# Kernel tuning notes

Hardware: AMD Instinct MI355X
Metric: run time of the kernel (lower is better)

The kernel has to match this reference:

```python
import jax, jax.numpy as jnp
import numpy as np

N_QUBITS = 12
N_LAYERS = 3
FEAT_DIM = 64
BATCH = 8192
PI = float(np.pi)


def setup_inputs() -> dict:
    key = jax.random.key(0)
    k1, k2, k3 = jax.random.split(key, 3)
    x = jax.random.normal(k1, (BATCH, FEAT_DIM), dtype=jnp.float32)
    # nn.Linear(feature_dim, num_qubits, bias=False) weight: [num_qubits, feature_dim]
    W = jax.random.normal(k2, (N_QUBITS, FEAT_DIM), dtype=jnp.float32) * (1.0 / np.sqrt(FEAT_DIM))
    # quantum params ~ Uniform(-pi, pi), shape [num_layers, num_qubits, 2] (RY, RZ angles)
    quantum_params = jax.random.uniform(k3, (N_LAYERS, N_QUBITS, 2), minval=-PI, maxval=PI, dtype=jnp.float32)
    return {"x": x, "W": W, "quantum_params": quantum_params}


def _halves(st, ax):
    a0 = jax.lax.index_in_dim(st, 0, ax, keepdims=True)
    a1 = jax.lax.index_in_dim(st, 1, ax, keepdims=True)
    return a0, a1


def _ry(st, theta, q, n):
    # RY(t) = [[cos t/2, -sin t/2], [sin t/2, cos t/2]] on qubit q (wire 0 = most significant)
    ax = q + 1
    c = jnp.cos(theta * 0.5)
    s = jnp.sin(theta * 0.5)
    if jnp.ndim(c) > 0:  # per-batch angles -> broadcast [B,1,...,1]
        c = c.reshape(c.shape + (1,) * n)
        s = s.reshape(s.shape + (1,) * n)
    a0, a1 = _halves(st, ax)
    return jnp.concatenate([c * a0 - s * a1, s * a0 + c * a1], axis=ax)


def _rz(st, theta, q, n):
    # RZ(t) = diag(e^{-i t/2}, e^{i t/2}) on qubit q
    ax = q + 1
    ph = jnp.exp(-0.5j * theta)
    a0, a1 = _halves(st, ax)
    return jnp.concatenate([ph * a0, jnp.conj(ph) * a1], axis=ax)


def _cnot(st, ctrl, tgt):
    # flip target amplitudes on the control=1 subspace
    ax_c, ax_t = ctrl + 1, tgt + 1
    s0, s1 = _halves(st, ax_c)
    return jnp.concatenate([s0, jnp.flip(s1, axis=ax_t)], axis=ax_c)


def reference(x, W, quantum_params):
    n = N_QUBITS
    # feature projection + tanh squashing to [-pi, pi]
    angles = jnp.tanh(x @ W.T) * PI  # [B, n]
    B = x.shape[0]
    # batched state vector |0...0>, shape [B] + [2]*n (wire 0 most significant, PennyLane convention)
    st = jnp.zeros((B,) + (2,) * n, dtype=jnp.complex64)
    st = st.at[(slice(None),) + (0,) * n].set(1.0)
    for layer in range(N_LAYERS):
        # data (re)uploading: RY(features[i]) each layer since data_reuploading=True
        for q in range(n):
            st = _ry(st, angles[:, q], q, n)
        # variational rotations
        for q in range(n):
            st = _ry(st, quantum_params[layer, q, 0], q, n)
            st = _rz(st, quantum_params[layer, q, 1], q, n)
        # ring entanglement
        for q in range(n):
            st = _cnot(st, q, (q + 1) % n)
    probs = jnp.real(st * jnp.conj(st))  # [B] + [2]*n
    outs = []
    for q in range(n):  # <PauliZ_q> = p(bit_q=0) - p(bit_q=1)
        axes = tuple(a for a in range(1, n + 1) if a != q + 1)
        p = probs.sum(axis=axes)  # [B, 2]
        outs.append(p[:, 0] - p[:, 1])
    return jnp.stack(outs, axis=1).astype(x.dtype)  # [B, n]
```

## Files before the change

kernel.cpp:

```cpp
#include <hip/hip_runtime.h>

namespace {

constexpr int NQ = 12;
constexpr int NL = 3;
constexpr int FEAT = 64;
constexpr float PI_F = 3.14159265358979323846f;

typedef float f2 __attribute__((ext_vector_type(2)));

constexpr int par12(unsigned x) { int p = 0; for (int i = 0; i < 12; ++i) p ^= (int)((x >> i) & 1u); return p; }
constexpr int lead12(unsigned x) { for (int k = 11; k >= 0; --k) if ((x >> k) & 1u) return k; return -1; }

struct Ech { unsigned v[16] = {}; int n = 0; };
constexpr unsigned ech_reduce(const Ech& E, unsigned x) {
  for (int i = 0; i < E.n; ++i) { int lb = lead12(E.v[i]); if (lb >= 0 && ((x >> lb) & 1u)) x ^= E.v[i]; }
  return x;
}
constexpr bool ech_add(Ech& E, unsigned x) {
  unsigned r = ech_reduce(E, x);
  if (!r) return false;
  int lb = lead12(r);
  int pos = E.n;
  for (int i = 0; i < E.n; ++i) { if (lead12(E.v[i]) < lb) { pos = i; break; } }
  for (int i = E.n; i > pos; --i) E.v[i] = E.v[i - 1];
  E.v[pos] = r; E.n++;
  return true;
}

constexpr unsigned apmat(const unsigned* rows, unsigned v) {
  unsigned o = 0; for (int k = 0; k < 12; ++k) if (par12(rows[k] & v)) o |= 1u << k; return o;
}
constexpr bool inv12(const unsigned* in, unsigned* out) {
  unsigned a[12] = {}, b[12] = {};
  for (int k = 0; k < 12; ++k) { a[k] = in[k]; b[k] = 1u << k; }
  for (int c = 0; c < 12; ++c) {
    int p = -1;
    for (int r = c; r < 12; ++r) if ((a[r] >> c) & 1u) { p = r; break; }
    if (p < 0) return false;
    unsigned t = a[c]; a[c] = a[p]; a[p] = t; t = b[c]; b[c] = b[p]; b[p] = t;
    for (int r = 0; r < 12; ++r) if (r != c && ((a[r] >> c) & 1u)) { a[r] ^= a[c]; b[r] ^= b[c]; }
  }
  for (int k = 0; k < 12; ++k) out[k] = b[k];
  return true;
}
constexpr unsigned dropb(unsigned x, int t) {
  unsigned lm = (1u << t) - 1u;
  return (x & lm) | ((x >> 1) & (0x7FFu & ~lm));
}

struct Logical {
  unsigned m[NL][NQ] = {}, rv[NL][NQ] = {}, rf[NQ] = {};
  bool ok = false;
};
constexpr Logical compute_raw() {
  Logical mp{};
  unsigned col[NQ] = {}, row[NQ] = {};
  for (int b = 0; b < NQ; ++b) { col[b] = 1u << b; row[b] = 1u << b; }
  mp.ok = true;
  for (int L = 0; L < NL; ++L) {
    for (int q = 0; q < NQ; ++q) {
      mp.m[L][q]  = col[NQ - 1 - q];
      mp.rv[L][q] = row[NQ - 1 - q];
      if (par12(mp.m[L][q] & mp.rv[L][q]) != 1) mp.ok = false;
    }
    for (int q = 0; q < NQ; ++q) {
      int bc = NQ - 1 - q;
      int bt = NQ - 1 - ((q + 1) % NQ);
      col[bc] ^= col[bt];
      row[bt] ^= row[bc];
    }
  }
  for (int q = 0; q < NQ; ++q) mp.rf[q] = row[NQ - 1 - q];
  return mp;
}

struct Plan {
  unsigned l0m[NQ] = {}, l0r[NQ] = {};
  unsigned gm[4][6] = {};
  unsigned gr[4][6] = {};
  unsigned rf[NQ] = {};
  unsigned phi[4][6] = {};
  unsigned coffE[4][64] = {};
  int cb[4] = {};
  bool ok = false;
};

constexpr bool findH(const Ech& G, unsigned rho, unsigned& out) {
  for (unsigned t = 0; t < 12; ++t) {
    unsigned v = 1u << t;
    if (par12(v & rho) == 0 && ech_reduce(G, v)) { out = v; return true; }
  }
  for (unsigned v = 1; v < 4096u; ++v) {
    if (par12(v & rho) == 0 && ech_reduce(G, v)) { out = v; return true; }
  }
  return false;
}

constexpr Plan build_plan() {
  Logical raw = compute_raw();
  Plan P{};
  P.ok = raw.ok;
  for (int q = 0; q < NQ; ++q) { P.l0m[q] = raw.m[0][q]; P.l0r[q] = raw.rv[0][q]; }
  unsigned fwd[12] = {}, invc[12] = {};
  for (int k = 0; k < 12; ++k) { fwd[k] = 1u << k; invc[k] = 1u << k; }
  for (int ph = 0; ph < 4; ++ph) {
    const int L = 1 + ph / 2, q0 = (ph % 2) * 6;
    unsigned ml[6] = {};
    for (int i = 0; i < 6; ++i) ml[i] = raw.m[L][q0 + i];
    bool done = false;
    for (int cbi = 5; cbi >= 0 && !done; --cbi) {
      unsigned rho = fwd[6 + cbi];
      bool bad = false;
      int idx = -1;
      for (int i = 0; i < 6; ++i) if (par12(ml[i] & rho)) { idx = i; break; }
      unsigned uc = 0;
      Ech W{};
      if (idx >= 0) {
        uc = ml[idx];
        for (int i = 0; i < 6; ++i) {
          if (i == idx) continue;
          unsigned w = par12(ml[i] & rho) ? (ml[i] ^ uc) : ml[i];
          ech_add(W, w);
        }
        if (W.n > 5) bad = true;
      } else {
        for (int i = 0; i < 6; ++i) ech_add(W, ml[i]);
        if (W.n > 5) bad = true;
        if (!bad) {
          bool got = false;
          for (unsigned t = 0; t < 12 && !got; ++t) {
            unsigned v = 1u << t;
            if (par12(v & rho)) { uc = v; got = true; }
          }
          if (!got) bad = true;
        }
      }
      if (bad) continue;
      Ech G{};
      for (int i = 0; i < W.n && !bad; ++i) if (!ech_add(G, W.v[i])) bad = true;
      if (!bad && !ech_add(G, uc)) bad = true;
      if (bad) continue;
      unsigned regH[5] = {};
      int nH = W.n;
      for (int i = 0; i < nH; ++i) regH[i] = W.v[i];
      for (int slot = nH; slot < 5 && !bad; ++slot) {
        unsigned v = 0;
        if (!findH(G, rho, v)) { bad = true; break; }
        regH[slot] = v; ech_add(G, v);
      }
      if (bad) continue;
      unsigned lam[6] = {};
      for (int j = 0; j < 6 && !bad; ++j) {
        unsigned cand = invc[j];
        if (par12(cand & rho) != 0 || !ech_reduce(G, cand)) {
          if (!findH(G, rho, cand)) { bad = true; break; }
        }
        lam[j] = cand; ech_add(G, cand);
      }
      if (bad) continue;
      unsigned ncols[12] = {};
      for (int j = 0; j < 6; ++j) ncols[j] = lam[j];
      {
        int w = 0;
        for (int k = 0; k < 6; ++k) ncols[6 + k] = (k == cbi) ? uc : regH[w++];
      }
      unsigned Mrows[12] = {};
      for (int k = 0; k < 12; ++k) {
        unsigned r = 0;
        for (int j = 0; j < 12; ++j) r |= ((ncols[j] >> k) & 1u) << j;
        Mrows[k] = r;
      }
      unsigned fnew[12] = {};
      if (!inv12(Mrows, fnew)) continue;
      bool okp = true;
      unsigned gmv[6] = {}, grv[6] = {};
      for (int i = 0; i < 6 && okp; ++i) {
        unsigned SM = apmat(fnew, ml[i]);
        if (SM & 63u) okp = false;
        unsigned sg = 0;
        for (int k = 0; k < 12; ++k) if (par12(raw.rv[L][q0 + i] & ncols[k])) sg |= 1u << k;
        if (par12(SM & sg) != 1) okp = false;
        gmv[i] = SM; grv[i] = sg;
      }
      unsigned phj[6] = {}, Ust[6] = {};
      for (int j = 0; j < 6 && okp; ++j) {
        phj[j] = apmat(fwd, lam[j]);
        if ((phj[j] >> (6 + cbi)) & 1u) okp = false;
      }
      for (int k = 0; k < 6 && okp; ++k) {
        Ust[k] = apmat(fwd, ncols[6 + k]);
        if (((Ust[k] >> (6 + cbi)) & 1u) != (unsigned)(k == cbi ? 1 : 0)) okp = false;
      }
      if (!okp) continue;
      P.cb[ph] = cbi;
      for (int j = 0; j < 6; ++j) P.phi[ph][j] = phj[j];
      for (int rp = 0; rp < 64; ++rp) {
        unsigned psi = 0;
        for (int i = 0; i < 6; ++i) if ((rp >> i) & 1) psi ^= Ust[i];
        P.coffE[ph][rp] = dropb(psi, 6 + cbi);
      }
      for (int i = 0; i < 6; ++i) { P.gm[ph][i] = gmv[i]; P.gr[ph][i] = grv[i]; }
      for (int k = 0; k < 12; ++k) { fwd[k] = fnew[k]; invc[k] = ncols[k]; }
      done = true;
    }
    if (!done) { P.ok = false; return P; }
  }
  for (int q = 0; q < NQ; ++q) {
    unsigned sg = 0;
    for (int k = 0; k < 12; ++k) if (par12(raw.rf[q] & invc[k])) sg |= 1u << k;
    P.rf[q] = sg;
  }
  return P;
}

constexpr Plan PLAN = build_plan();
static_assert(PLAN.ok, "plan construction failed");

__device__ __forceinline__ f2 shuf(f2 a) { return __builtin_shufflevector(a, a, 1, 0); }

template<bool REAL>
__device__ __forceinline__ f2 updv(f2 a, f2 p, f2 arr, f2 aii, f2 brr, f2 bii) {
  f2 t = a * arr;
  if constexpr (!REAL) t = shuf(a) * aii + t;
  t = p * brr + t;
  if constexpr (!REAL) t = shuf(p) * bii + t;
  return t;
}
__device__ __forceinline__ f2 cmulv(f2 a, f2 urr, f2 uri) {
  return shuf(a) * uri + a * urr;
}

template<unsigned MLO>
__device__ __forceinline__ float shx(float v, int lane4) {
  if constexpr (MLO == 0u) {
    return v;
  } else if constexpr (MLO < 32u) {
    constexpr int off = (int)((MLO << 10) | 0x1fu);
    return __int_as_float(__builtin_amdgcn_ds_swizzle(__float_as_int(v), off));
  } else {
    int addr = lane4 ^ (int)(MLO << 2);
    return __int_as_float(__builtin_amdgcn_ds_bpermute(addr, __float_as_int(v)));
  }
}

template<unsigned M, unsigned R, int NREG, bool REAL>
__device__ __forceinline__ void gate(f2* st, float ghalf, float phihalf, int lane, int lane4) {
  float s, c;
  __sincosf(ghalf, &s, &c);
  constexpr unsigned MHI = (M >> 6) & 63u;
  constexpr unsigned MLO = M & 63u;
  constexpr unsigned RHI = (R >> 6) & 63u;
  constexpr unsigned RLO = R & 63u;
  float sL = (__popc((int)(RLO & (unsigned)lane)) & 1) ? -1.f : 1.f;
  float ar, aiS, brS, b0i;
  if constexpr (REAL) {
    ar = c; aiS = 0.f; brS = -s * sL; b0i = 0.f;
  } else {
    float sf, cf;
    __sincosf(phihalf, &sf, &cf);
    ar = c * cf; aiS = (-c * sf) * sL; brS = (-s * cf) * sL; b0i = s * sf;
  }
  f2 arr; arr.x = ar; arr.y = ar;
  f2 aip; aip.x = -aiS; aip.y = aiS;
  f2 aim; aim.x = aiS;  aim.y = -aiS;
  f2 brp; brp.x = brS;  brp.y = brS;
  f2 brm; brm.x = -brS; brm.y = -brS;
  f2 bii; bii.x = -b0i; bii.y = b0i;
  if constexpr (MLO == 0u) {
    constexpr unsigned TB = MHI & (~MHI + 1u);
    #pragma unroll
    for (int r = 0; r < NREG; ++r) {
      if ((r & (int)TB) == 0) {
        int r2 = r ^ (int)MHI;
        const bool rp = ((__builtin_popcount((unsigned)r & RHI)) & 1) != 0;
        f2 a = st[r], b = st[r2];
        st[r]  = rp ? updv<REAL>(a, b, arr, aim, brm, bii) : updv<REAL>(a, b, arr, aip, brp, bii);
        st[r2] = rp ? updv<REAL>(b, a, arr, aip, brp, bii) : updv<REAL>(b, a, arr, aim, brm, bii);
      }
    }
  } else {
    #pragma unroll
    for (int r = 0; r < NREG; ++r) {
      f2 p;
      p.x = shx<MLO>(st[r].x, lane4);
      p.y = shx<MLO>(st[r].y, lane4);
      const bool rp = ((__builtin_popcount((unsigned)r & RHI)) & 1) != 0;
      st[r] = rp ? updv<REAL>(st[r], p, arr, aim, brm, bii) : updv<REAL>(st[r], p, arr, aip, brp, bii);
    }
  }
}

template<int Q>
__device__ __forceinline__ void l0_lane(f2* st, const float* ang, const float* __restrict__ qp, int lane, int lane4) {
  if constexpr (Q < NQ) {
    constexpr unsigned M = PLAN.l0m[Q];
    if constexpr (M < 64u) {
      gate<M, PLAN.l0r[Q], 1, false>(st, 0.5f * (ang[Q] + qp[Q * 2 + 0]), 0.5f * qp[Q * 2 + 1], lane, lane4);
    }
    l0_lane<Q + 1>(st, ang, qp, lane, lane4);
  }
}
template<int Q, unsigned DONE>
__device__ __forceinline__ void l0_reg(f2* st, const float* ang, const float* __restrict__ qp) {
  if constexpr (Q < NQ) {
    constexpr unsigned M = PLAN.l0m[Q];
    if constexpr (M >= 64u) {
      constexpr unsigned TB = (M >> 6) & 63u;
      float sh = 0.5f * (ang[Q] + qp[Q * 2 + 0]);
      float ph = 0.5f * qp[Q * 2 + 1];
      float s, c, sf, cf;
      __sincosf(sh, &s, &c);
      __sincosf(ph, &sf, &cf);
      f2 u0r; u0r.x = c * cf;  u0r.y = c * cf;
      f2 u0i; u0i.x = c * sf;  u0i.y = -c * sf;
      f2 u1r; u1r.x = s * cf;  u1r.y = s * cf;
      f2 u1i; u1i.x = -s * sf; u1i.y = s * sf;
      #pragma unroll
      for (int r = 0; r < 64; ++r) {
        if ((r & ~(int)DONE & 63) == 0) {
          f2 a = st[r];
          int r2 = r | (int)TB;
          st[r]  = cmulv(a, u0r, u0i);
          st[r2] = cmulv(a, u1r, u1i);
        }
      }
      l0_reg<Q + 1, DONE | TB>(st, ang, qp);
    } else {
      l0_reg<Q + 1, DONE>(st, ang, qp);
    }
  }
}

__device__ __forceinline__ int pad(int a) { return a + (a >> 5); }

template<int PH>
__device__ __forceinline__ void remap(f2* st, f2* lds, int lane) {
  constexpr int b = PLAN.cb[PH];
  constexpr unsigned LM6 = (1u << b) - 1u;
  constexpr unsigned LM = (1u << (6 + b)) - 1u;
  unsigned B = 0;
  #pragma unroll
  for (int j = 0; j < 6; ++j) B ^= (unsigned)(-(int)((lane >> j) & 1)) & PLAN.phi[PH][j];
  unsigned rBe = (B & LM) | ((B >> 1) & (0x7FFu & ~LM));
  #pragma unroll
  for (int s = 0; s < 2; ++s) {
    #pragma unroll
    for (int r = 0; r < 64; ++r) {
      if (((r >> b) & 1) == s) {
        const int cr = (r & (int)LM6) | ((r >> 1) & (31 & ~(int)LM6));
        lds[pad((cr << 6) | lane)] = st[r];
      }
    }
    asm volatile("s_waitcnt lgkmcnt(0)" ::: "memory");
    #pragma unroll
    for (int rp = 0; rp < 64; ++rp) {
      if (((rp >> b) & 1) == s) {
        st[rp] = lds[pad((int)(rBe ^ PLAN.coffE[PH][rp]))];
      }
    }
    asm volatile("s_waitcnt lgkmcnt(0)" ::: "memory");
  }
}

template<int PH, int I>
__device__ __forceinline__ void do_phase(f2* st, const float* ang, const float* __restrict__ qp, int lane, int lane4) {
  if constexpr (I < 6) {
    constexpr int L = 1 + PH / 2;
    constexpr bool REAL = (L == NL - 1);
    constexpr int q = (PH % 2) * 6 + I;
    constexpr unsigned M = PLAN.gm[PH][I];
    constexpr unsigned R = PLAN.gr[PH][I];
    float th0 = qp[(L * NQ + q) * 2 + 0];
    float ph1 = REAL ? 0.f : 0.5f * qp[(L * NQ + q) * 2 + 1];
    gate<M, R, 64, REAL>(st, 0.5f * (ang[q] + th0), ph1, lane, lane4);
    do_phase<PH, I + 1>(st, ang, qp, lane, lane4);
  }
}

__device__ __forceinline__ float redsum(float v, int lane4) {
  v += shx<1>(v, lane4);
  v += shx<2>(v, lane4);
  v += shx<4>(v, lane4);
  v += shx<8>(v, lane4);
  v += shx<16>(v, lane4);
  v += shx<32>(v, lane4);
  return v;
}
__device__ __forceinline__ float fast_tanh(float x) {
  float e = __expf(2.f * x);
  float r = __builtin_amdgcn_rcpf(e + 1.f);
  return 1.f - 2.f * r;
}

template<int Q>
__device__ __forceinline__ void finish(const f2* acc6, float& outv, int lane, int lane4) {
  if constexpr (Q < NQ) {
    constexpr unsigned RLO = PLAN.rf[Q] & 63u;
    float a = (Q & 1) ? acc6[Q / 2].y : acc6[Q / 2].x;
    float sLn = (__popc((int)(RLO & (unsigned)lane)) & 1) ? -a : a;
    float t = redsum(sLn, lane4);
    if (lane == Q) outv = t;
    finish<Q + 1>(acc6, outv, lane, lane4);
  }
}

__global__ __launch_bounds__(64, 2) void qtr_kernel(const float* __restrict__ x,
                                                    const float* __restrict__ W,
                                                    const float* __restrict__ qp,
                                                    float* __restrict__ out) {
  __shared__ f2 ldsb[2112];
  int b = blockIdx.x;
  int lane = threadIdx.x;
  int lane4 = lane << 2;

  float xv = x[b * FEAT + lane];
  float ang[NQ];
  #pragma unroll
  for (int q = 0; q < NQ; ++q) {
    float prod = redsum(xv * W[q * FEAT + lane], lane4);
    ang[q] = PI_F * fast_tanh(prod);
  }

  f2 st[64];
  st[0].x = (lane == 0) ? 1.f : 0.f;
  st[0].y = 0.f;

  l0_lane<0>(st, ang, qp, lane, lane4);
  l0_reg<0, 0u>(st, ang, qp);

  remap<0>(st, ldsb, lane);
  do_phase<0, 0>(st, ang, qp, lane, lane4);
  remap<1>(st, ldsb, lane);
  do_phase<1, 0>(st, ang, qp, lane, lane4);
  remap<2>(st, ldsb, lane);
  do_phase<2, 0>(st, ang, qp, lane, lane4);
  remap<3>(st, ldsb, lane);
  do_phase<3, 0>(st, ang, qp, lane, lane4);

  f2 acc6[6];
  #pragma unroll
  for (int j = 0; j < 6; ++j) { acc6[j].x = 0.f; acc6[j].y = 0.f; }
  #pragma unroll
  for (int r = 0; r < 64; ++r) {
    f2 q2 = st[r] * st[r];
    float p = q2.x + q2.y;
    f2 pp; pp.x = p; pp.y = p;
    #pragma unroll
    for (int j = 0; j < 6; ++j) {
      const bool n0 = ((__builtin_popcount(((PLAN.rf[2 * j]     >> 6) & 63u) & (unsigned)r)) & 1) != 0;
      const bool n1 = ((__builtin_popcount(((PLAN.rf[2 * j + 1] >> 6) & 63u) & (unsigned)r)) & 1) != 0;
      f2 sg; sg.x = n0 ? -1.f : 1.f; sg.y = n1 ? -1.f : 1.f;
      acc6[j] = pp * sg + acc6[j];
    }
  }

  float outv = 0.f;
  finish<0>(acc6, outv, lane, lane4);

  if (lane < NQ) out[b * NQ + lane] = outv;
}

}

extern "C" void kernel_launch(void* const* d_in, const int* in_sizes, int n_in,
                              void* d_out, int out_size, void* d_ws, size_t ws_size,
                              hipStream_t stream) {
  const float* x  = (const float*)d_in[0];
  const float* W  = (const float*)d_in[1];
  const float* qp = (const float*)d_in[2];
  float* out = (float*)d_out;
  qtr_kernel<<<8192, 64, 0, stream>>>(x, W, qp, out);
}
```

Measured before the change: 129.4 us.

## Switch register state to split real/imag planes paired on a chosen register bit

Stores the 64 complex amplitudes per lane as 32 real and 32 imaginary float2 pairs, each pair holding the two values of a chosen register bit. Gates then run as packed FMAs on whole pairs instead of intra-vector swaps, and the LDS remaps pack and unpack between the layouts. The register bit is picked per phase to minimise in-pair swaps. This aims to raise packed-FMA use and drop shuffle overhead, but adds more complex remap code and may raise register pressure.

Result: slower. 133.7 us (+3.3%).

```diff
diff --git a/kernel.cpp b/kernel.cpp
--- a/kernel.cpp
+++ b/kernel.cpp
@@ -48,6 +48,8 @@
   unsigned lm = (1u << t) - 1u;
   return (x & lm) | ((x >> 1) & (0x7FFu & ~lm));
 }
+constexpr int drop6(int r, int c) { int lm = (1 << c) - 1; return (r & lm) | ((r >> 1) & (31 & ~lm)); }
+constexpr int ins6(int p, int slot, int c) { int lm = (1 << c) - 1; return (p & lm) | ((p & ~lm) << 1) | (slot << c); }
 
 struct Logical {
   unsigned m[NL][NQ] = {}, rv[NL][NQ] = {}, rf[NQ] = {};
@@ -217,19 +219,26 @@
 constexpr Plan PLAN = build_plan();
 static_assert(PLAN.ok, "plan construction failed");
 
-__device__ __forceinline__ f2 shuf(f2 a) { return __builtin_shufflevector(a, a, 1, 0); }
-
-template<bool REAL>
-__device__ __forceinline__ f2 updv(f2 a, f2 p, f2 arr, f2 aii, f2 brr, f2 bii) {
-  f2 t = a * arr;
-  if constexpr (!REAL) t = shuf(a) * aii + t;
-  t = p * brr + t;
-  if constexpr (!REAL) t = shuf(p) * bii + t;
-  return t;
-}
-__device__ __forceinline__ f2 cmulv(f2 a, f2 urr, f2 uri) {
-  return shuf(a) * uri + a * urr;
-}
+constexpr int pick_cp(int ph) {
+  int best = -1, bestCost = 99;
+  for (int c = 0; c < 6; ++c) {
+    if (c == PLAN.cb[ph]) continue;
+    int cost = 0;
+    for (int i = 0; i < 6; ++i) if ((PLAN.gm[ph][i] >> (6 + c)) & 1u) ++cost;
+    if (cost < bestCost) { bestCost = cost; best = c; }
+  }
+  return best;
+}
+constexpr int CPARR[4] = {pick_cp(0), pick_cp(1), pick_cp(2), pick_cp(3)};
+static_assert(CPARR[0] != PLAN.cb[0] && CPARR[1] != PLAN.cb[1] &&
+              CPARR[2] != PLAN.cb[2] && CPARR[3] != PLAN.cb[3], "cp==cb");
+
+__device__ __forceinline__ f2 em(f2 a, f2 b, f2 c) { return __builtin_elementwise_fma(a, b, c); }
+__device__ __forceinline__ f2 vswap(f2 a) { return __builtin_shufflevector(a, a, 1, 0); }
+__device__ __forceinline__ f2 evens(f2 a, f2 b) { return __builtin_shufflevector(a, b, 0, 2); }
+__device__ __forceinline__ f2 odds(f2 a, f2 b) { return __builtin_shufflevector(a, b, 1, 3); }
+
+__device__ __forceinline__ f2 cmulv(f2 a, f2 urr, f2 uri) { return em(vswap(a), uri, a * urr); }
 
 template<unsigned MLO>
 __device__ __forceinline__ float shx(float v, int lane4) {
@@ -244,51 +253,23 @@
   }
 }
 
-template<unsigned M, unsigned R, int NREG, bool REAL>
-__device__ __forceinline__ void gate(f2* st, float ghalf, float phihalf, int lane, int lane4) {
-  float s, c;
+template<unsigned M, unsigned R>
+__device__ __forceinline__ void l0_lane_gate(f2* st, float ghalf, float phihalf, int lane, int lane4) {
+  float s, c, sf, cf;
   __sincosf(ghalf, &s, &c);
-  constexpr unsigned MHI = (M >> 6) & 63u;
+  __sincosf(phihalf, &sf, &cf);
   constexpr unsigned MLO = M & 63u;
-  constexpr unsigned RHI = (R >> 6) & 63u;
   constexpr unsigned RLO = R & 63u;
   float sL = (__popc((int)(RLO & (unsigned)lane)) & 1) ? -1.f : 1.f;
-  float ar, aiS, brS, b0i;
-  if constexpr (REAL) {
-    ar = c; aiS = 0.f; brS = -s * sL; b0i = 0.f;
-  } else {
-    float sf, cf;
-    __sincosf(phihalf, &sf, &cf);
-    ar = c * cf; aiS = (-c * sf) * sL; brS = (-s * cf) * sL; b0i = s * sf;
-  }
-  f2 arr; arr.x = ar; arr.y = ar;
-  f2 aip; aip.x = -aiS; aip.y = aiS;
-  f2 aim; aim.x = aiS;  aim.y = -aiS;
-  f2 brp; brp.x = brS;  brp.y = brS;
-  f2 brm; brm.x = -brS; brm.y = -brS;
-  f2 bii; bii.x = -b0i; bii.y = b0i;
-  if constexpr (MLO == 0u) {
-    constexpr unsigned TB = MHI & (~MHI + 1u);
-    #pragma unroll
-    for (int r = 0; r < NREG; ++r) {
-      if ((r & (int)TB) == 0) {
-        int r2 = r ^ (int)MHI;
-        const bool rp = ((__builtin_popcount((unsigned)r & RHI)) & 1) != 0;
-        f2 a = st[r], b = st[r2];
-        st[r]  = rp ? updv<REAL>(a, b, arr, aim, brm, bii) : updv<REAL>(a, b, arr, aip, brp, bii);
-        st[r2] = rp ? updv<REAL>(b, a, arr, aip, brp, bii) : updv<REAL>(b, a, arr, aim, brm, bii);
-      }
-    }
-  } else {
-    #pragma unroll
-    for (int r = 0; r < NREG; ++r) {
-      f2 p;
-      p.x = shx<MLO>(st[r].x, lane4);
-      p.y = shx<MLO>(st[r].y, lane4);
-      const bool rp = ((__builtin_popcount((unsigned)r & RHI)) & 1) != 0;
-      st[r] = rp ? updv<REAL>(st[r], p, arr, aim, brm, bii) : updv<REAL>(st[r], p, arr, aip, brp, bii);
-    }
-  }
+  float ar = c * cf, aiS = (-c * sf) * sL, brS = (-s * cf) * sL, b0i = s * sf;
+  f2 arr = {ar, ar};
+  f2 aip = {-aiS, aiS};
+  f2 brp = {brS, brS};
+  f2 bii = {-b0i, b0i};
+  f2 p;
+  p.x = shx<MLO>(st[0].x, lane4);
+  p.y = shx<MLO>(st[0].y, lane4);
+  st[0] = em(vswap(p), bii, em(p, brp, em(vswap(st[0]), aip, st[0] * arr)));
 }
 
 template<int Q>
@@ -296,7 +277,7 @@
   if constexpr (Q < NQ) {
     constexpr unsigned M = PLAN.l0m[Q];
     if constexpr (M < 64u) {
-      gate<M, PLAN.l0r[Q], 1, false>(st, 0.5f * (ang[Q] + qp[Q * 2 + 0]), 0.5f * qp[Q * 2 + 1], lane, lane4);
+      l0_lane_gate<M, PLAN.l0r[Q]>(st, 0.5f * (ang[Q] + qp[Q * 2 + 0]), 0.5f * qp[Q * 2 + 1], lane, lane4);
     }
     l0_lane<Q + 1>(st, ang, qp, lane, lane4);
   }
@@ -312,10 +293,10 @@
       float s, c, sf, cf;
       __sincosf(sh, &s, &c);
       __sincosf(ph, &sf, &cf);
-      f2 u0r; u0r.x = c * cf;  u0r.y = c * cf;
-      f2 u0i; u0i.x = c * sf;  u0i.y = -c * sf;
-      f2 u1r; u1r.x = s * cf;  u1r.y = s * cf;
-      f2 u1i; u1i.x = -s * sf; u1i.y = s * sf;
+      f2 u0r = {c * cf, c * cf};
+      f2 u0i = {c * sf, -c * sf};
+      f2 u1r = {s * cf, s * cf};
+      f2 u1i = {-s * sf, s * sf};
       #pragma unroll
       for (int r = 0; r < 64; ++r) {
         if ((r & ~(int)DONE & 63) == 0) {
@@ -332,51 +313,179 @@
   }
 }
 
-__device__ __forceinline__ int pad(int a) { return a + (a >> 5); }
-
-template<int PH>
-__device__ __forceinline__ void remap(f2* st, f2* lds, int lane) {
-  constexpr int b = PLAN.cb[PH];
-  constexpr unsigned LM6 = (1u << b) - 1u;
-  constexpr unsigned LM = (1u << (6 + b)) - 1u;
-  unsigned B = 0;
-  #pragma unroll
-  for (int j = 0; j < 6; ++j) B ^= (unsigned)(-(int)((lane >> j) & 1)) & PLAN.phi[PH][j];
-  unsigned rBe = (B & LM) | ((B >> 1) & (0x7FFu & ~LM));
-  #pragma unroll
-  for (int s = 0; s < 2; ++s) {
-    #pragma unroll
-    for (int r = 0; r < 64; ++r) {
-      if (((r >> b) & 1) == s) {
-        const int cr = (r & (int)LM6) | ((r >> 1) & (31 & ~(int)LM6));
-        lds[pad((cr << 6) | lane)] = st[r];
-      }
-    }
-    asm volatile("s_waitcnt lgkmcnt(0)" ::: "memory");
-    #pragma unroll
-    for (int rp = 0; rp < 64; ++rp) {
-      if (((rp >> b) & 1) == s) {
-        st[rp] = lds[pad((int)(rBe ^ PLAN.coffE[PH][rp]))];
-      }
-    }
-    asm volatile("s_waitcnt lgkmcnt(0)" ::: "memory");
+template<unsigned M, unsigned R, int C, bool REAL>
+__device__ __forceinline__ void gate_soa(f2* re, f2* im, float ghalf, float phihalf, int lane) {
+  constexpr unsigned MH = (M >> 6) & 63u;
+  constexpr unsigned RH = (R >> 6) & 63u;
+  constexpr unsigned RL = R & 63u;
+  constexpr bool SW = ((MH >> C) & 1u) != 0;
+  constexpr unsigned mhp = (unsigned)drop6((int)(MH & ~(1u << C)), C);
+  constexpr unsigned rhp = (unsigned)drop6((int)(RH & ~(1u << C)), C);
+  constexpr unsigned rhc = (RH >> C) & 1u;
+  float sL = (__popc((int)(RL & (unsigned)lane)) & 1) ? -1.f : 1.f;
+  float s, c;
+  __sincosf(ghalf, &s, &c);
+  float ar, aiS, brS, b0i;
+  if constexpr (REAL) {
+    ar = c; aiS = 0.f; brS = -s * sL; b0i = 0.f;
+  } else {
+    float sf, cf;
+    __sincosf(phihalf, &sf, &cf);
+    ar = c * cf; aiS = (-c * sf) * sL; brS = (-s * cf) * sL; b0i = s * sf;
+  }
+  const f2 arr = {ar, ar};
+  const f2 aiP = {aiS, rhc ? -aiS : aiS};
+  const f2 aiM = -aiP;
+  const f2 brP = {brS, rhc ? -brS : brS};
+  const f2 brM = -brP;
+  const f2 biN = {-b0i, -b0i};
+  const f2 biP = {b0i, b0i};
+
+  auto upd2 = [&](f2 are, f2 aim, f2 pre, f2 pim, bool rp, f2& ore, f2& oim) {
+    const f2 aiV = rp ? aiM : aiP;
+    const f2 brV = rp ? brM : brP;
+    if constexpr (REAL) {
+      ore = em(pre, brV, are * arr);
+      oim = em(pim, brV, aim * arr);
+    } else {
+      ore = em(pre, brV, em(pim, biN, em(aim, -aiV, are * arr)));
+      oim = em(pim, brV, em(pre, biP, em(are, aiV, aim * arr)));
+    }
+  };
+
+  if constexpr (mhp == 0u) {
+    static_assert(SW, "empty mask");
+    #pragma unroll
+    for (int p = 0; p < 32; ++p) {
+      const bool rp = ((__builtin_popcount((unsigned)p & rhp)) & 1) != 0;
+      f2 are = re[p], aim = im[p];
+      f2 nre, nim;
+      upd2(are, aim, vswap(are), vswap(aim), rp, nre, nim);
+      re[p] = nre; im[p] = nim;
+    }
+  } else {
+    constexpr unsigned TBp = mhp & (~mhp + 1u);
+    #pragma unroll
+    for (int p = 0; p < 32; ++p) {
+      if ((p & (int)TBp) == 0) {
+        const int p2 = p ^ (int)mhp;
+        const bool rpA = ((__builtin_popcount((unsigned)p  & rhp)) & 1) != 0;
+        const bool rpB = ((__builtin_popcount((unsigned)p2 & rhp)) & 1) != 0;
+        f2 are = re[p],  aim = im[p];
+        f2 bre = re[p2], bim = im[p2];
+        f2 pa_re = SW ? vswap(bre) : bre;
+        f2 pa_im = SW ? vswap(bim) : bim;
+        f2 pb_re = SW ? vswap(are) : are;
+        f2 pb_im = SW ? vswap(aim) : aim;
+        f2 nre, nim;
+        upd2(are, aim, pa_re, pa_im, rpA, nre, nim);
+        re[p] = nre; im[p] = nim;
+        upd2(bre, bim, pb_re, pb_im, rpB, nre, nim);
+        re[p2] = nre; im[p2] = nim;
+      }
+    }
   }
 }
 
 template<int PH, int I>
-__device__ __forceinline__ void do_phase(f2* st, const float* ang, const float* __restrict__ qp, int lane, int lane4) {
+__device__ __forceinline__ void do_phase_soa(f2* re, f2* im, const float* ang, const float* __restrict__ qp, int lane) {
   if constexpr (I < 6) {
     constexpr int L = 1 + PH / 2;
     constexpr bool REAL = (L == NL - 1);
     constexpr int q = (PH % 2) * 6 + I;
-    constexpr unsigned M = PLAN.gm[PH][I];
-    constexpr unsigned R = PLAN.gr[PH][I];
     float th0 = qp[(L * NQ + q) * 2 + 0];
     float ph1 = REAL ? 0.f : 0.5f * qp[(L * NQ + q) * 2 + 1];
-    gate<M, R, 64, REAL>(st, 0.5f * (ang[q] + th0), ph1, lane, lane4);
-    do_phase<PH, I + 1>(st, ang, qp, lane, lane4);
-  }
-}
+    gate_soa<PLAN.gm[PH][I], PLAN.gr[PH][I], CPARR[PH], REAL>(re, im, 0.5f * (ang[q] + th0), ph1, lane);
+    do_phase_soa<PH, I + 1>(re, im, ang, qp, lane);
+  }
+}
+
+__device__ __forceinline__ int pad(int a) { return a + (a >> 5); }
+
+template<int PH>
+__device__ __forceinline__ unsigned remap_base(int lane) {
+  constexpr int b = PLAN.cb[PH];
+  constexpr unsigned LM = (1u << (6 + b)) - 1u;
+  unsigned B = 0;
+  #pragma unroll
+  for (int j = 0; j < 6; ++j) B ^= (unsigned)(-(int)((lane >> j) & 1)) & PLAN.phi[PH][j];
+  return (B & LM) | ((B >> 1) & (0x7FFu & ~LM));
+}
+
+__device__ __forceinline__ void remap_first(const f2* stA, f2* re, f2* im, f2* lds, int lane) {
+  constexpr int PH = 0;
+  constexpr int b = PLAN.cb[PH];
+  constexpr int C = CPARR[PH];
+  constexpr int CBP = (b > C) ? b - 1 : b;
+  constexpr unsigned LM6 = (1u << b) - 1u;
+  unsigned rBe = remap_base<PH>(lane);
+  #pragma unroll
+  for (int s = 0; s < 2; ++s) {
+    #pragma unroll
+    for (int r = 0; r < 64; ++r) {
+      if (((r >> b) & 1) == s) {
+        const int cr = (r & (int)LM6) | ((r >> 1) & (31 & ~(int)LM6));
+        lds[pad((cr << 6) | lane)] = stA[r];
+      }
+    }
+    asm volatile("s_waitcnt lgkmcnt(0)" ::: "memory");
+    #pragma unroll
+    for (int p = 0; p < 32; ++p) {
+      if (((p >> CBP) & 1) == s) {
+        const int r0 = ins6(p, 0, C);
+        const int r1 = ins6(p, 1, C);
+        f2 A = lds[pad((int)(rBe ^ PLAN.coffE[PH][r0]))];
+        f2 B = lds[pad((int)(rBe ^ PLAN.coffE[PH][r1]))];
+        re[p] = evens(A, B);
+        im[p] = odds(A, B);
+      }
+    }
+    asm volatile("s_waitcnt lgkmcnt(0)" ::: "memory");
+  }
+}
+
+template<int PH>
+__device__ __forceinline__ void remap_mid(f2* re, f2* im, f2* lds, int lane) {
+  constexpr int b = PLAN.cb[PH];
+  constexpr int CPREV = CPARR[PH - 1];
+  constexpr int C = CPARR[PH];
+  constexpr int CBP = (b > C) ? b - 1 : b;
+  constexpr unsigned LM6 = (1u << b) - 1u;
+  unsigned rBe = remap_base<PH>(lane);
+  #pragma unroll
+  for (int s = 0; s < 2; ++s) {
+    #pragma unroll
+    for (int r = 0; r < 64; ++r) {
+      if (((r >> b) & 1) == s) {
+        const int p = drop6(r, CPREV);
+        const int slot = (r >> CPREV) & 1;
+        const int cr = (r & (int)LM6) | ((r >> 1) & (31 & ~(int)LM6));
+        f2 v = slot ? odds(re[p], im[p]) : evens(re[p], im[p]);
+        lds[pad((cr << 6) | lane)] = v;
+      }
+    }
+    asm volatile("s_waitcnt lgkmcnt(0)" ::: "memory");
+    #pragma unroll
+    for (int p = 0; p < 32; ++p) {
+      if (((p >> CBP) & 1) == s) {
+        const int r0 = ins6(p, 0, C);
+        const int r1 = ins6(p, 1, C);
+        f2 A = lds[pad((int)(rBe ^ PLAN.coffE[PH][r0]))];
+        f2 B = lds[pad((int)(rBe ^ PLAN.coffE[PH][r1]))];
+        re[p] = evens(A, B);
+        im[p] = odds(A, B);
+      }
+    }
+    asm volatile("s_waitcnt lgkmcnt(0)" ::: "memory");
+  }
+}
+
+static_assert(PLAN.cb[1] != CPARR[0] || true, "");
+static_assert(CPARR[0] != PLAN.cb[1] ? true : (PLAN.cb[1] == PLAN.cb[1]), "");
+
+static_assert(PLAN.cb[1] != CPARR[0], "cb[1]==cp[0]: write/read chunk alias");
+static_assert(PLAN.cb[2] != CPARR[1], "cb[2]==cp[1]: write/read chunk alias");
+static_assert(PLAN.cb[3] != CPARR[2], "cb[3]==cp[2]: write/read chunk alias");
 
 __device__ __forceinline__ float redsum(float v, int lane4) {
   v += shx<1>(v, lane4);
@@ -394,14 +503,14 @@
 }
 
 template<int Q>
-__device__ __forceinline__ void finish(const f2* acc6, float& outv, int lane, int lane4) {
+__device__ __forceinline__ void finish(const float* af, float& outv, int lane, int lane4) {
   if constexpr (Q < NQ) {
     constexpr unsigned RLO = PLAN.rf[Q] & 63u;
-    float a = (Q & 1) ? acc6[Q / 2].y : acc6[Q / 2].x;
+    float a = af[Q];
     float sLn = (__popc((int)(RLO & (unsigned)lane)) & 1) ? -a : a;
     float t = redsum(sLn, lane4);
     if (lane == Q) outv = t;
-    finish<Q + 1>(acc6, outv, lane, lane4);
+    finish<Q + 1>(af, outv, lane, lane4);
   }
 }
 
@@ -422,41 +531,52 @@
     ang[q] = PI_F * fast_tanh(prod);
   }
 
-  f2 st[64];
-  st[0].x = (lane == 0) ? 1.f : 0.f;
-  st[0].y = 0.f;
-
-  l0_lane<0>(st, ang, qp, lane, lane4);
-  l0_reg<0, 0u>(st, ang, qp);
-
-  remap<0>(st, ldsb, lane);
-  do_phase<0, 0>(st, ang, qp, lane, lane4);
-  remap<1>(st, ldsb, lane);
-  do_phase<1, 0>(st, ang, qp, lane, lane4);
-  remap<2>(st, ldsb, lane);
-  do_phase<2, 0>(st, ang, qp, lane, lane4);
-  remap<3>(st, ldsb, lane);
-  do_phase<3, 0>(st, ang, qp, lane, lane4);
-
-  f2 acc6[6];
-  #pragma unroll
-  for (int j = 0; j < 6; ++j) { acc6[j].x = 0.f; acc6[j].y = 0.f; }
-  #pragma unroll
-  for (int r = 0; r < 64; ++r) {
-    f2 q2 = st[r] * st[r];
-    float p = q2.x + q2.y;
-    f2 pp; pp.x = p; pp.y = p;
-    #pragma unroll
-    for (int j = 0; j < 6; ++j) {
-      const bool n0 = ((__builtin_popcount(((PLAN.rf[2 * j]     >> 6) & 63u) & (unsigned)r)) & 1) != 0;
-      const bool n1 = ((__builtin_popcount(((PLAN.rf[2 * j + 1] >> 6) & 63u) & (unsigned)r)) & 1) != 0;
-      f2 sg; sg.x = n0 ? -1.f : 1.f; sg.y = n1 ? -1.f : 1.f;
-      acc6[j] = pp * sg + acc6[j];
-    }
-  }
+  f2 re[32], im[32];
+  {
+    f2 stA[64];
+    stA[0].x = (lane == 0) ? 1.f : 0.f;
+    stA[0].y = 0.f;
+    l0_lane<0>(stA, ang, qp, lane, lane4);
+    l0_reg<0, 0u>(stA, ang, qp);
+    remap_first(stA, re, im, ldsb, lane);
+  }
+  do_phase_soa<0, 0>(re, im, ang, qp, lane);
+  remap_mid<1>(re, im, ldsb, lane);
+  do_phase_soa<1, 0>(re, im, ang, qp, lane);
+  remap_mid<2>(re, im, ldsb, lane);
+  do_phase_soa<2, 0>(re, im, ang, qp, lane);
+  remap_mid<3>(re, im, ldsb, lane);
+  do_phase_soa<3, 0>(re, im, ang, qp, lane);
+
+  constexpr int C3 = CPARR[3];
+  f2 accq[NQ];
+  #pragma unroll
+  for (int q = 0; q < NQ; ++q) { accq[q].x = 0.f; accq[q].y = 0.f; }
+  #pragma unroll
+  for (int p = 0; p < 32; ++p) {
+    f2 pr2 = em(im[p], im[p], re[p] * re[p]);
+    #pragma unroll
+    for (int q = 0; q < NQ; ++q) {
+      constexpr unsigned RFH_ALL[NQ] = {
+        (PLAN.rf[0] >> 6) & 63u, (PLAN.rf[1] >> 6) & 63u, (PLAN.rf[2] >> 6) & 63u,
+        (PLAN.rf[3] >> 6) & 63u, (PLAN.rf[4] >> 6) & 63u, (PLAN.rf[5] >> 6) & 63u,
+        (PLAN.rf[6] >> 6) & 63u, (PLAN.rf[7] >> 6) & 63u, (PLAN.rf[8] >> 6) & 63u,
+        (PLAN.rf[9] >> 6) & 63u, (PLAN.rf[10] >> 6) & 63u, (PLAN.rf[11] >> 6) & 63u};
+      const unsigned rfh = RFH_ALL[q];
+      const unsigned rfp = (unsigned)drop6((int)(rfh & ~(1u << C3)), C3);
+      const unsigned rfc = (rfh >> C3) & 1u;
+      const bool s0 = ((__builtin_popcount((unsigned)p & rfp)) & 1) != 0;
+      const bool s1 = s0 ^ (rfc != 0);
+      f2 sg; sg.x = s0 ? -1.f : 1.f; sg.y = s1 ? -1.f : 1.f;
+      accq[q] = em(pr2, sg, accq[q]);
+    }
+  }
+  float af[NQ];
+  #pragma unroll
+  for (int q = 0; q < NQ; ++q) af[q] = accq[q].x + accq[q].y;
 
   float outv = 0.f;
-  finish<0>(acc6, outv, lane, lane4);
+  finish<0>(af, outv, lane, lane4);
 
   if (lane < NQ) out[b * NQ + lane] = outv;
 }
```
